# Performance work log

Measured on AMD Instinct MI355X. Metric: run time of the kernel, lower is better.

## Reference

```python
import jax, jax.numpy as jnp
import numpy as np

N, E, D, ATT = 20000, 5000, 128, 32
NUM_LAYERS = 4
LN_EPS = 1e-5
DEG_EPS = 1e-12

def setup_inputs() -> dict:
    key = jax.random.key(0)
    k1, k2, k3, k4 = jax.random.split(key, 4)
    node_embeddings = jax.random.normal(k1, (N, D), dtype=jnp.float32)
    hypergraph_matrix = (jax.random.uniform(k2, (N, E)) < 0.01).astype(jnp.float32)
    ln_gamma = jnp.ones((D,), jnp.float32)
    ln_beta = jnp.zeros((D,), jnp.float32)
    W_att = jax.random.normal(k3, (D, ATT), dtype=jnp.float32) * (1.0 / np.sqrt(D))
    b_att = jnp.zeros((ATT,), jnp.float32)
    q_att = jax.random.normal(k4, (ATT,), dtype=jnp.float32)
    return {"node_embeddings": node_embeddings, "hypergraph_matrix": hypergraph_matrix,
            "ln_gamma": ln_gamma, "ln_beta": ln_beta,
            "W_att": W_att, "b_att": b_att, "q_att": q_att}

def _layernorm(y, gamma, beta):
    mu = jnp.mean(y, axis=-1, keepdims=True)
    var = jnp.mean(jnp.square(y - mu), axis=-1, keepdims=True)
    return (y - mu) * jax.lax.rsqrt(var + LN_EPS) * gamma + beta

def reference(node_embeddings, hypergraph_matrix, ln_gamma, ln_beta, W_att, b_att, q_att):
    H = hypergraph_matrix                      # [N, E]
    dv_inv = 1.0 / jnp.maximum(jnp.sum(H, axis=1), DEG_EPS)   # [N]
    de_inv = 1.0 / jnp.maximum(jnp.sum(H, axis=0), DEG_EPS)   # [E]
    x = node_embeddings
    for _ in range(NUM_LAYERS):
        edge_mean = (H.T @ x) * de_inv[:, None]       # V->E mean, [E, D]
        node_msg = (H @ edge_mean) * dv_inv[:, None]  # E->V mean, [N, D]
        x = _layernorm(node_msg + node_embeddings, ln_gamma, ln_beta)
        # dropout(p=0.35) is identity in eval mode
    # per-edge masked mean over member nodes (vectorized segment-mean)
    M = (H > 0).astype(x.dtype)                        # [N, E]
    cnt = jnp.maximum(jnp.sum(M, axis=0), 1.0)         # [E]
    edge_out = (M.T @ x) / cnt[:, None]                # [E, D]
    # dot-product attention pooling over hyperedges
    scores = jax.nn.softmax(jnp.tanh(edge_out @ W_att + b_att) @ q_att)  # [E]
    return scores @ edge_out                           # [D]
```

## Files before the change

kernel.cpp:

```cpp
#include <hip/hip_runtime.h>
#include <hip/hip_bf16.h>
#include <hip/hip_fp16.h>
#include <math.h>

#define NN 20000
#define EE 5000
#define DD 128
#define ATT 32
#define NUM_LAYERS 4
#define LN_EPS 1e-5f
#define DEG_EPS 1e-12f

#define ECAP 320
#define NCAP 128

__device__ inline void acc4h(float4& a, uint2 u) {
    __half2 h0 = __builtin_bit_cast(__half2, u.x);
    __half2 h1 = __builtin_bit_cast(__half2, u.y);
    a.x += __low2float(h0); a.y += __high2float(h0);
    a.z += __low2float(h1); a.w += __high2float(h1);
}

__device__ inline uint2 pack4h(float x, float y, float z, float w) {
    uint2 u;
    u.x = __builtin_bit_cast(unsigned, __floats2half2_rn(x, y));
    u.y = __builtin_bit_cast(unsigned, __floats2half2_rn(z, w));
    return u;
}

__global__ __launch_bounds__(256) void build_lists(
    const float* __restrict__ H, int* __restrict__ ec, int* __restrict__ nc,
    int* __restrict__ el, int* __restrict__ nl) {
    const int n = blockIdx.x;
    const int tid = threadIdx.x;
    __shared__ int lcnt;
    if (tid == 0) lcnt = 0;
    __syncthreads();
    const float4* row = reinterpret_cast<const float4*>(H + (size_t)n * EE);
    for (int i = tid; i < EE / 4; i += 256) {
        float4 h = row[i];
        float v[4] = {h.x, h.y, h.z, h.w};
        const int ebase = i * 4;
#pragma unroll
        for (int k = 0; k < 4; k++) {
            if (v[k] != 0.0f) {
                const int e = ebase + k;
                int s = atomicAdd(&lcnt, 1);
                if (s < NCAP) nl[n * NCAP + s] = e;
                int se = atomicAdd(&ec[e], 1);
                if (se < ECAP) el[e * ECAP + se] = n;
            }
        }
    }
    __syncthreads();
    if (tid == 0) nc[n] = lcnt;
}

__global__ __launch_bounds__(256) void cvt_to_h(
    const float* __restrict__ src, __half* __restrict__ dst, int n4) {
    const int i = blockIdx.x * 256 + threadIdx.x;
    if (i >= n4) return;
    const float4 v = reinterpret_cast<const float4*>(src)[i];
    reinterpret_cast<uint2*>(dst)[i] = pack4h(v.x, v.y, v.z, v.w);
}

template <bool OUT_HALF>
__global__ __launch_bounds__(256) void edge_gather(
    const __half* __restrict__ xh, const int* __restrict__ ec,
    const int* __restrict__ el, void* __restrict__ out) {
    __shared__ float4 part[4][32];
    const int e = blockIdx.x;
    const int tid = threadIdx.x;
    const int wv = tid >> 6;
    const int lane = tid & 63;
    const int q = lane & 31;
    const int stream = wv * 2 + (lane >> 5);
    const int cnt = ec[e];
    const int c = min(cnt, ECAP);
    const int* lst = el + e * ECAP;
    float4 a0 = make_float4(0.f, 0.f, 0.f, 0.f);
    float4 a1 = make_float4(0.f, 0.f, 0.f, 0.f);
    int i = stream;
    for (; i + 8 < c; i += 16) {
        const int n0 = lst[i];
        const int n1 = lst[i + 8];
        const uint2 r0 = *reinterpret_cast<const uint2*>(xh + n0 * DD + (q << 2));
        const uint2 r1 = *reinterpret_cast<const uint2*>(xh + n1 * DD + (q << 2));
        acc4h(a0, r0);
        acc4h(a1, r1);
    }
    if (i < c) {
        const uint2 r0 = *reinterpret_cast<const uint2*>(xh + lst[i] * DD + (q << 2));
        acc4h(a0, r0);
    }
    a0.x += a1.x; a0.y += a1.y; a0.z += a1.z; a0.w += a1.w;
    a0.x += __shfl_down(a0.x, 32);
    a0.y += __shfl_down(a0.y, 32);
    a0.z += __shfl_down(a0.z, 32);
    a0.w += __shfl_down(a0.w, 32);
    if (lane < 32) part[wv][q] = a0;
    __syncthreads();
    if (tid < 32) {
        const float4 p0 = part[0][q];
        const float4 p1 = part[1][q];
        const float4 p2 = part[2][q];
        const float4 p3 = part[3][q];
        const float inv = 1.0f / fmaxf((float)cnt, DEG_EPS);
        const float ox = (p0.x + p1.x + p2.x + p3.x) * inv;
        const float oy = (p0.y + p1.y + p2.y + p3.y) * inv;
        const float oz = (p0.z + p1.z + p2.z + p3.z) * inv;
        const float ow = (p0.w + p1.w + p2.w + p3.w) * inv;
        if (OUT_HALF) {
            reinterpret_cast<uint2*>((__half*)out + e * DD)[q] = pack4h(ox, oy, oz, ow);
        } else {
            reinterpret_cast<float4*>((float*)out + e * DD)[q] = make_float4(ox, oy, oz, ow);
        }
    }
}

__global__ __launch_bounds__(128) void node_gather_ln(
    const __half* __restrict__ emean, const int* __restrict__ nc,
    const int* __restrict__ nl, const float* __restrict__ x0,
    const float* __restrict__ gamma, const float* __restrict__ beta,
    __half* __restrict__ xout) {
    __shared__ float4 part[2][32];
    const int n = blockIdx.x;
    const int tid = threadIdx.x;
    const int wv = tid >> 6;
    const int lane = tid & 63;
    const int q = lane & 31;
    const int stream = wv * 2 + (lane >> 5);
    const int cnt = nc[n];
    const int c = min(cnt, NCAP);
    const int* lst = nl + n * NCAP;
    float4 a0 = make_float4(0.f, 0.f, 0.f, 0.f);
    float4 a1 = make_float4(0.f, 0.f, 0.f, 0.f);
    int i = stream;
    for (; i + 4 < c; i += 8) {
        const int e0 = lst[i];
        const int e1 = lst[i + 4];
        const uint2 r0 = *reinterpret_cast<const uint2*>(emean + e0 * DD + (q << 2));
        const uint2 r1 = *reinterpret_cast<const uint2*>(emean + e1 * DD + (q << 2));
        acc4h(a0, r0);
        acc4h(a1, r1);
    }
    if (i < c) {
        const uint2 r0 = *reinterpret_cast<const uint2*>(emean + lst[i] * DD + (q << 2));
        acc4h(a0, r0);
    }
    a0.x += a1.x; a0.y += a1.y; a0.z += a1.z; a0.w += a1.w;
    a0.x += __shfl_down(a0.x, 32);
    a0.y += __shfl_down(a0.y, 32);
    a0.z += __shfl_down(a0.z, 32);
    a0.w += __shfl_down(a0.w, 32);
    if (lane < 32) part[wv][q] = a0;
    __syncthreads();
    if (tid < 64) {
        const float4 p0 = part[0][q];
        const float4 p1 = part[1][q];
        const float inv = 1.0f / fmaxf((float)cnt, DEG_EPS);
        const float4 x0v = *reinterpret_cast<const float4*>(x0 + n * DD + (q << 2));
        float4 y;
        y.x = (p0.x + p1.x) * inv + x0v.x;
        y.y = (p0.y + p1.y) * inv + x0v.y;
        y.z = (p0.z + p1.z) * inv + x0v.z;
        y.w = (p0.w + p1.w) * inv + x0v.w;
        float s = y.x + y.y + y.z + y.w;
        float ss = y.x * y.x + y.y * y.y + y.z * y.z + y.w * y.w;
        for (int off = 16; off > 0; off >>= 1) {
            s += __shfl_down(s, off);
            ss += __shfl_down(ss, off);
        }
        s = __shfl(s, 0);
        ss = __shfl(ss, 0);
        const float mu = s * (1.0f / 128.0f);
        float var = ss * (1.0f / 128.0f) - mu * mu;
        var = fmaxf(var, 0.0f);
        const float rstd = 1.0f / sqrtf(var + LN_EPS);
        if (lane < 32) {
            const float4 g = *reinterpret_cast<const float4*>(gamma + (q << 2));
            const float4 b = *reinterpret_cast<const float4*>(beta + (q << 2));
            const float ox = (y.x - mu) * rstd * g.x + b.x;
            const float oy = (y.y - mu) * rstd * g.y + b.y;
            const float oz = (y.z - mu) * rstd * g.z + b.z;
            const float ow = (y.w - mu) * rstd * g.w + b.w;
            reinterpret_cast<uint2*>(xout + n * DD)[q] = pack4h(ox, oy, oz, ow);
        }
    }
}

__global__ __launch_bounds__(128) void att_scores(
    const float* __restrict__ eout, const float* __restrict__ W,
    const float* __restrict__ b, const float* __restrict__ qv,
    float* __restrict__ t) {
    __shared__ float row[DD];
    const int e = blockIdx.x;
    const int tid = threadIdx.x;
    row[tid] = eout[e * DD + tid];
    __syncthreads();
    float r = 0.0f;
    if (tid < ATT) {
        float a = 0.0f;
#pragma unroll 4
        for (int d = 0; d < DD; d++) a += row[d] * W[d * ATT + tid];
        r = tanhf(a + b[tid]) * qv[tid];
    }
    for (int off = 16; off > 0; off >>= 1) r += __shfl_down(r, off);
    if (tid == 0) t[e] = r;
}

__global__ __launch_bounds__(1024) void softmax_stats(
    const float* __restrict__ t, float* __restrict__ MS) {
    __shared__ float red[16];
    __shared__ float smax;
    const int tid = threadIdx.x;
    const int wid = tid >> 6;
    float m = -1e30f;
    for (int i = tid; i < EE; i += 1024) m = fmaxf(m, t[i]);
    for (int off = 32; off > 0; off >>= 1) m = fmaxf(m, __shfl_down(m, off));
    if ((tid & 63) == 0) red[wid] = m;
    __syncthreads();
    if (tid < 64) {
        float v = (tid < 16) ? red[tid] : -1e30f;
        for (int off = 8; off > 0; off >>= 1) v = fmaxf(v, __shfl_down(v, off));
        if (tid == 0) smax = v;
    }
    __syncthreads();
    const float M = smax;
    float sum = 0.0f;
    for (int i = tid; i < EE; i += 1024) sum += expf(t[i] - M);
    for (int off = 32; off > 0; off >>= 1) sum += __shfl_down(sum, off);
    if ((tid & 63) == 0) red[wid] = sum;
    __syncthreads();
    if (tid < 64) {
        float v = (tid < 16) ? red[tid] : 0.0f;
        for (int off = 8; off > 0; off >>= 1) v += __shfl_down(v, off);
        if (tid == 0) { MS[0] = M; MS[1] = v; }
    }
}

__global__ __launch_bounds__(128) void weighted_sum(
    const float* __restrict__ eout, const float* __restrict__ t,
    const float* __restrict__ MS, float* __restrict__ out) {
    const int d = threadIdx.x;
    const float M = MS[0];
    const float invS = 1.0f / MS[1];
    float acc = 0.0f;
    for (int e = blockIdx.x; e < EE; e += gridDim.x) {
        const float w = expf(t[e] - M);
        acc += w * eout[e * DD + d];
    }
    atomicAdd(&out[d], acc * invS);
}

extern "C" void kernel_launch(void* const* d_in, const int* in_sizes, int n_in,
                              void* d_out, int out_size, void* d_ws, size_t ws_size,
                              hipStream_t stream) {
    const float* x0 = (const float*)d_in[0];
    const float* H = (const float*)d_in[1];
    const float* gamma = (const float*)d_in[2];
    const float* beta = (const float*)d_in[3];
    const float* W = (const float*)d_in[4];
    const float* b = (const float*)d_in[5];
    const float* qv = (const float*)d_in[6];
    float* out = (float*)d_out;

    char* w = (char*)d_ws;
    int* ec = (int*)w;       w += (size_t)EE * 4;
    int* nc = (int*)w;       w += (size_t)NN * 4;
    int* el = (int*)w;       w += (size_t)EE * ECAP * 4;
    int* nl = (int*)w;       w += (size_t)NN * NCAP * 4;
    __half* xh0 = (__half*)w; w += (size_t)NN * DD * 2;
    __half* xA = (__half*)w;  w += (size_t)NN * DD * 2;
    __half* xB = (__half*)w;  w += (size_t)NN * DD * 2;
    __half* emean = (__half*)w; w += (size_t)EE * DD * 2;
    float* eout = (float*)w; w += (size_t)EE * DD * 4;
    float* t = (float*)w;    w += (size_t)EE * 4;
    float* MS = (float*)w;   w += 16;

    hipMemsetAsync(d_ws, 0, (size_t)(EE + NN) * 4, stream);
    hipMemsetAsync(d_out, 0, (size_t)DD * sizeof(float), stream);

    build_lists<<<NN, 256, 0, stream>>>(H, ec, nc, el, nl);
    cvt_to_h<<<(NN * DD / 4 + 255) / 256, 256, 0, stream>>>(x0, xh0, NN * DD / 4);

    const __half* xin = xh0;
    __half* bufs[2] = {xA, xB};
    for (int l = 0; l < NUM_LAYERS; l++) {
        edge_gather<true><<<EE, 256, 0, stream>>>(xin, ec, el, emean);
        node_gather_ln<<<NN, 128, 0, stream>>>(emean, nc, nl, x0, gamma, beta, bufs[l & 1]);
        xin = bufs[l & 1];
    }

    edge_gather<false><<<EE, 256, 0, stream>>>(xin, ec, el, eout);
    att_scores<<<EE, 128, 0, stream>>>(eout, W, b, qv, t);
    softmax_stats<<<1, 1024, 0, stream>>>(t, MS);
    weighted_sum<<<64, 128, 0, stream>>>(eout, t, MS, out);
}
```

Before: 911.5 us.

## Split incidence list build into row and column passes, widen gathers to 16-byte loads

The single list-building kernel, which did global atomics per nonzero for the edge lists, becomes two kernels. A row pass builds node lists in shared memory. A column pass scans 16-column strips in 4 row chunks and builds edge lists with shared atomics plus one global atomic per column per chunk. The gather kernels now stage index lists in shared memory and use 16-byte half loads (8 features per lane), and the final edge gather is fused with the attention-score computation to drop a launch and an eout reread. The column pass reads H with strided 64-byte row segments, which may be less efficient, and H is now read twice.

```diff
diff --git a/kernel.cpp b/kernel.cpp
--- a/kernel.cpp
+++ b/kernel.cpp
@@ -1,5 +1,4 @@
 #include <hip/hip_runtime.h>
-#include <hip/hip_bf16.h>
 #include <hip/hip_fp16.h>
 #include <math.h>
 
@@ -14,26 +13,28 @@
 #define ECAP 320
 #define NCAP 128
 
-__device__ inline void acc4h(float4& a, uint2 u) {
-    __half2 h0 = __builtin_bit_cast(__half2, u.x);
-    __half2 h1 = __builtin_bit_cast(__half2, u.y);
-    a.x += __low2float(h0); a.y += __high2float(h0);
-    a.z += __low2float(h1); a.w += __high2float(h1);
-}
-
-__device__ inline uint2 pack4h(float x, float y, float z, float w) {
-    uint2 u;
-    u.x = __builtin_bit_cast(unsigned, __floats2half2_rn(x, y));
-    u.y = __builtin_bit_cast(unsigned, __floats2half2_rn(z, w));
-    return u;
-}
-
-__global__ __launch_bounds__(256) void build_lists(
-    const float* __restrict__ H, int* __restrict__ ec, int* __restrict__ nc,
-    int* __restrict__ el, int* __restrict__ nl) {
+#define CP_COLS 16
+#define CP_ROWCHUNK 5000
+#define CP_NCHUNKS ((EE + CP_COLS - 1) / CP_COLS)
+#define CP_CAP 128
+
+__device__ inline unsigned pack2h(float x, float y) {
+    return __builtin_bit_cast(unsigned, __floats2half2_rn(x, y));
+}
+__device__ inline void acc8(float* a, uint4 u) {
+    __half2 h;
+    h = __builtin_bit_cast(__half2, u.x); a[0] += __low2float(h); a[1] += __high2float(h);
+    h = __builtin_bit_cast(__half2, u.y); a[2] += __low2float(h); a[3] += __high2float(h);
+    h = __builtin_bit_cast(__half2, u.z); a[4] += __low2float(h); a[5] += __high2float(h);
+    h = __builtin_bit_cast(__half2, u.w); a[6] += __low2float(h); a[7] += __high2float(h);
+}
+
+__global__ __launch_bounds__(256) void rowpass_nl(
+    const float* __restrict__ H, int* __restrict__ nc, int* __restrict__ nl) {
     const int n = blockIdx.x;
     const int tid = threadIdx.x;
     __shared__ int lcnt;
+    __shared__ int lbuf[NCAP];
     if (tid == 0) lcnt = 0;
     __syncthreads();
     const float4* row = reinterpret_cast<const float4*>(H + (size_t)n * EE);
@@ -44,16 +45,65 @@
 #pragma unroll
         for (int k = 0; k < 4; k++) {
             if (v[k] != 0.0f) {
-                const int e = ebase + k;
                 int s = atomicAdd(&lcnt, 1);
-                if (s < NCAP) nl[n * NCAP + s] = e;
-                int se = atomicAdd(&ec[e], 1);
-                if (se < ECAP) el[e * ECAP + se] = n;
+                if (s < NCAP) lbuf[s] = ebase + k;
             }
         }
     }
     __syncthreads();
+    const int c = min(lcnt, NCAP);
+    for (int k = tid; k < c; k += 256) nl[(size_t)n * NCAP + k] = lbuf[k];
     if (tid == 0) nc[n] = lcnt;
+}
+
+__global__ __launch_bounds__(256) void colpass_el(
+    const float* __restrict__ H, int* __restrict__ ec, int* __restrict__ el) {
+    const int cchunk = blockIdx.x % CP_NCHUNKS;
+    const int rchunk = blockIdx.x / CP_NCHUNKS;
+    const int cbase = cchunk * CP_COLS;
+    const int cw = min(CP_COLS, EE - cbase);
+    const int r0 = rchunk * CP_ROWCHUNK;
+    __shared__ int lcnt[CP_COLS];
+    __shared__ int lbase[CP_COLS];
+    __shared__ int lists[CP_COLS][CP_CAP];
+    const int tid = threadIdx.x;
+    if (tid < CP_COLS) lcnt[tid] = 0;
+    __syncthreads();
+    for (int r = tid; r < CP_ROWCHUNK; r += 256) {
+        const int row = r0 + r;
+        const float* p = H + (size_t)row * EE + cbase;
+        float v[CP_COLS];
+        *reinterpret_cast<float4*>(v + 0) = *reinterpret_cast<const float4*>(p + 0);
+        *reinterpret_cast<float4*>(v + 4) = *reinterpret_cast<const float4*>(p + 4);
+        if (cw == CP_COLS) {
+            *reinterpret_cast<float4*>(v + 8)  = *reinterpret_cast<const float4*>(p + 8);
+            *reinterpret_cast<float4*>(v + 12) = *reinterpret_cast<const float4*>(p + 12);
+        }
+#pragma unroll
+        for (int j = 0; j < CP_COLS; j++) {
+            if (j < cw && v[j] != 0.0f) {
+                int s = atomicAdd(&lcnt[j], 1);
+                if (s < CP_CAP) lists[j][s] = row;
+            }
+        }
+    }
+    __syncthreads();
+    const int j = tid >> 4;
+    const int k0 = tid & 15;
+    if (j < cw) {
+        const int cnt = min(lcnt[j], CP_CAP);
+        if (k0 == 0) lbase[j] = atomicAdd(&ec[cbase + j], cnt);
+    }
+    __syncthreads();
+    if (j < cw) {
+        const int cnt = min(lcnt[j], CP_CAP);
+        const int base = lbase[j];
+        int* dst = el + (size_t)(cbase + j) * ECAP;
+        for (int k = k0; k < cnt; k += 16) {
+            const int idx = base + k;
+            if (idx < ECAP) dst[idx] = lists[j][k];
+        }
+    }
 }
 
 __global__ __launch_bounds__(256) void cvt_to_h(
@@ -61,152 +111,169 @@
     const int i = blockIdx.x * 256 + threadIdx.x;
     if (i >= n4) return;
     const float4 v = reinterpret_cast<const float4*>(src)[i];
-    reinterpret_cast<uint2*>(dst)[i] = pack4h(v.x, v.y, v.z, v.w);
-}
-
-template <bool OUT_HALF>
-__global__ __launch_bounds__(256) void edge_gather(
+    uint2 u; u.x = pack2h(v.x, v.y); u.y = pack2h(v.z, v.w);
+    reinterpret_cast<uint2*>(dst)[i] = u;
+}
+
+template <bool FINAL>
+__global__ __launch_bounds__(256) void edge_gather16(
     const __half* __restrict__ xh, const int* __restrict__ ec,
-    const int* __restrict__ el, void* __restrict__ out) {
-    __shared__ float4 part[4][32];
+    const int* __restrict__ el, __half* __restrict__ outh,
+    float* __restrict__ eout, const float* __restrict__ W,
+    const float* __restrict__ bb, const float* __restrict__ qv,
+    float* __restrict__ t) {
+    __shared__ int ilst[ECAP];
+    __shared__ float part[4][16][8];
+    __shared__ float rowbuf[DD];
     const int e = blockIdx.x;
     const int tid = threadIdx.x;
-    const int wv = tid >> 6;
-    const int lane = tid & 63;
-    const int q = lane & 31;
-    const int stream = wv * 2 + (lane >> 5);
     const int cnt = ec[e];
     const int c = min(cnt, ECAP);
-    const int* lst = el + e * ECAP;
-    float4 a0 = make_float4(0.f, 0.f, 0.f, 0.f);
-    float4 a1 = make_float4(0.f, 0.f, 0.f, 0.f);
-    int i = stream;
-    for (; i + 8 < c; i += 16) {
-        const int n0 = lst[i];
-        const int n1 = lst[i + 8];
-        const uint2 r0 = *reinterpret_cast<const uint2*>(xh + n0 * DD + (q << 2));
-        const uint2 r1 = *reinterpret_cast<const uint2*>(xh + n1 * DD + (q << 2));
-        acc4h(a0, r0);
-        acc4h(a1, r1);
+    const int* lst = el + (size_t)e * ECAP;
+    for (int k = tid; k < c; k += 256) ilst[k] = lst[k];
+    __syncthreads();
+    const int lane16 = tid & 15;
+    const int s = tid >> 4;
+    const int wave = tid >> 6;
+    float a[8] = {0, 0, 0, 0, 0, 0, 0, 0};
+    float b[8] = {0, 0, 0, 0, 0, 0, 0, 0};
+    int i = s;
+    for (; i + 16 < c; i += 32) {
+        const int n0 = ilst[i];
+        const int n1 = ilst[i + 16];
+        acc8(a, *reinterpret_cast<const uint4*>(xh + n0 * DD + lane16 * 8));
+        acc8(b, *reinterpret_cast<const uint4*>(xh + n1 * DD + lane16 * 8));
     }
     if (i < c) {
-        const uint2 r0 = *reinterpret_cast<const uint2*>(xh + lst[i] * DD + (q << 2));
-        acc4h(a0, r0);
-    }
-    a0.x += a1.x; a0.y += a1.y; a0.z += a1.z; a0.w += a1.w;
-    a0.x += __shfl_down(a0.x, 32);
-    a0.y += __shfl_down(a0.y, 32);
-    a0.z += __shfl_down(a0.z, 32);
-    a0.w += __shfl_down(a0.w, 32);
-    if (lane < 32) part[wv][q] = a0;
-    __syncthreads();
-    if (tid < 32) {
-        const float4 p0 = part[0][q];
-        const float4 p1 = part[1][q];
-        const float4 p2 = part[2][q];
-        const float4 p3 = part[3][q];
+        acc8(a, *reinterpret_cast<const uint4*>(xh + ilst[i] * DD + lane16 * 8));
+    }
+#pragma unroll
+    for (int k = 0; k < 8; k++) {
+        float v = a[k] + b[k];
+        v += __shfl_down(v, 16);
+        v += __shfl_down(v, 32);
+        a[k] = v;
+    }
+    if ((tid & 63) < 16) {
+#pragma unroll
+        for (int k = 0; k < 8; k++) part[wave][lane16][k] = a[k];
+    }
+    __syncthreads();
+    if (tid < 16) {
         const float inv = 1.0f / fmaxf((float)cnt, DEG_EPS);
-        const float ox = (p0.x + p1.x + p2.x + p3.x) * inv;
-        const float oy = (p0.y + p1.y + p2.y + p3.y) * inv;
-        const float oz = (p0.z + p1.z + p2.z + p3.z) * inv;
-        const float ow = (p0.w + p1.w + p2.w + p3.w) * inv;
-        if (OUT_HALF) {
-            reinterpret_cast<uint2*>((__half*)out + e * DD)[q] = pack4h(ox, oy, oz, ow);
+        float o[8];
+#pragma unroll
+        for (int k = 0; k < 8; k++)
+            o[k] = (part[0][tid][k] + part[1][tid][k] + part[2][tid][k] + part[3][tid][k]) * inv;
+        if (!FINAL) {
+            uint4 u;
+            u.x = pack2h(o[0], o[1]); u.y = pack2h(o[2], o[3]);
+            u.z = pack2h(o[4], o[5]); u.w = pack2h(o[6], o[7]);
+            *reinterpret_cast<uint4*>(outh + e * DD + tid * 8) = u;
         } else {
-            reinterpret_cast<float4*>((float*)out + e * DD)[q] = make_float4(ox, oy, oz, ow);
-        }
-    }
-}
-
-__global__ __launch_bounds__(128) void node_gather_ln(
+#pragma unroll
+            for (int k = 0; k < 8; k++) rowbuf[tid * 8 + k] = o[k];
+            *reinterpret_cast<float4*>(eout + e * DD + tid * 8) =
+                make_float4(o[0], o[1], o[2], o[3]);
+            *reinterpret_cast<float4*>(eout + e * DD + tid * 8 + 4) =
+                make_float4(o[4], o[5], o[6], o[7]);
+        }
+    }
+    if (FINAL) {
+        __syncthreads();
+        float r = 0.0f;
+        if (tid < ATT) {
+            float acc = 0.0f;
+#pragma unroll 4
+            for (int d = 0; d < DD; d++) acc += rowbuf[d] * W[d * ATT + tid];
+            r = tanhf(acc + bb[tid]) * qv[tid];
+        }
+        for (int off = 16; off > 0; off >>= 1) r += __shfl_down(r, off);
+        if (tid == 0) t[e] = r;
+    }
+}
+
+__global__ __launch_bounds__(128) void node_gather_ln16(
     const __half* __restrict__ emean, const int* __restrict__ nc,
     const int* __restrict__ nl, const float* __restrict__ x0,
     const float* __restrict__ gamma, const float* __restrict__ beta,
     __half* __restrict__ xout) {
-    __shared__ float4 part[2][32];
+    __shared__ int ilst[NCAP];
+    __shared__ float part[2][16][8];
     const int n = blockIdx.x;
     const int tid = threadIdx.x;
-    const int wv = tid >> 6;
-    const int lane = tid & 63;
-    const int q = lane & 31;
-    const int stream = wv * 2 + (lane >> 5);
     const int cnt = nc[n];
     const int c = min(cnt, NCAP);
-    const int* lst = nl + n * NCAP;
-    float4 a0 = make_float4(0.f, 0.f, 0.f, 0.f);
-    float4 a1 = make_float4(0.f, 0.f, 0.f, 0.f);
-    int i = stream;
-    for (; i + 4 < c; i += 8) {
-        const int e0 = lst[i];
-        const int e1 = lst[i + 4];
-        const uint2 r0 = *reinterpret_cast<const uint2*>(emean + e0 * DD + (q << 2));
-        const uint2 r1 = *reinterpret_cast<const uint2*>(emean + e1 * DD + (q << 2));
-        acc4h(a0, r0);
-        acc4h(a1, r1);
+    const int* lst = nl + (size_t)n * NCAP;
+    if (tid < c) ilst[tid] = lst[tid];
+    __syncthreads();
+    const int lane16 = tid & 15;
+    const int s = tid >> 4;
+    const int wave = tid >> 6;
+    float a[8] = {0, 0, 0, 0, 0, 0, 0, 0};
+    float b[8] = {0, 0, 0, 0, 0, 0, 0, 0};
+    int i = s;
+    for (; i + 8 < c; i += 16) {
+        const int e0 = ilst[i];
+        const int e1 = ilst[i + 8];
+        acc8(a, *reinterpret_cast<const uint4*>(emean + e0 * DD + lane16 * 8));
+        acc8(b, *reinterpret_cast<const uint4*>(emean + e1 * DD + lane16 * 8));
     }
     if (i < c) {
-        const uint2 r0 = *reinterpret_cast<const uint2*>(emean + lst[i] * DD + (q << 2));
-        acc4h(a0, r0);
-    }
-    a0.x += a1.x; a0.y += a1.y; a0.z += a1.z; a0.w += a1.w;
-    a0.x += __shfl_down(a0.x, 32);
-    a0.y += __shfl_down(a0.y, 32);
-    a0.z += __shfl_down(a0.z, 32);
-    a0.w += __shfl_down(a0.w, 32);
-    if (lane < 32) part[wv][q] = a0;
-    __syncthreads();
-    if (tid < 64) {
-        const float4 p0 = part[0][q];
-        const float4 p1 = part[1][q];
+        acc8(a, *reinterpret_cast<const uint4*>(emean + ilst[i] * DD + lane16 * 8));
+    }
+#pragma unroll
+    for (int k = 0; k < 8; k++) {
+        float v = a[k] + b[k];
+        v += __shfl_down(v, 16);
+        v += __shfl_down(v, 32);
+        a[k] = v;
+    }
+    if ((tid & 63) < 16) {
+#pragma unroll
+        for (int k = 0; k < 8; k++) part[wave][lane16][k] = a[k];
+    }
+    __syncthreads();
+    if (tid < 16) {
         const float inv = 1.0f / fmaxf((float)cnt, DEG_EPS);
-        const float4 x0v = *reinterpret_cast<const float4*>(x0 + n * DD + (q << 2));
-        float4 y;
-        y.x = (p0.x + p1.x) * inv + x0v.x;
-        y.y = (p0.y + p1.y) * inv + x0v.y;
-        y.z = (p0.z + p1.z) * inv + x0v.z;
-        y.w = (p0.w + p1.w) * inv + x0v.w;
-        float s = y.x + y.y + y.z + y.w;
-        float ss = y.x * y.x + y.y * y.y + y.z * y.z + y.w * y.w;
-        for (int off = 16; off > 0; off >>= 1) {
-            s += __shfl_down(s, off);
+        const float4 x0a = *reinterpret_cast<const float4*>(x0 + n * DD + tid * 8);
+        const float4 x0b = *reinterpret_cast<const float4*>(x0 + n * DD + tid * 8 + 4);
+        float y[8];
+        y[0] = (part[0][tid][0] + part[1][tid][0]) * inv + x0a.x;
+        y[1] = (part[0][tid][1] + part[1][tid][1]) * inv + x0a.y;
+        y[2] = (part[0][tid][2] + part[1][tid][2]) * inv + x0a.z;
+        y[3] = (part[0][tid][3] + part[1][tid][3]) * inv + x0a.w;
+        y[4] = (part[0][tid][4] + part[1][tid][4]) * inv + x0b.x;
+        y[5] = (part[0][tid][5] + part[1][tid][5]) * inv + x0b.y;
+        y[6] = (part[0][tid][6] + part[1][tid][6]) * inv + x0b.z;
+        y[7] = (part[0][tid][7] + part[1][tid][7]) * inv + x0b.w;
+        float sm = 0.0f, ss = 0.0f;
+#pragma unroll
+        for (int k = 0; k < 8; k++) { sm += y[k]; ss += y[k] * y[k]; }
+        for (int off = 8; off > 0; off >>= 1) {
+            sm += __shfl_down(sm, off);
             ss += __shfl_down(ss, off);
         }
-        s = __shfl(s, 0);
+        sm = __shfl(sm, 0);
         ss = __shfl(ss, 0);
-        const float mu = s * (1.0f / 128.0f);
+        const float mu = sm * (1.0f / 128.0f);
         float var = ss * (1.0f / 128.0f) - mu * mu;
         var = fmaxf(var, 0.0f);
         const float rstd = 1.0f / sqrtf(var + LN_EPS);
-        if (lane < 32) {
-            const float4 g = *reinterpret_cast<const float4*>(gamma + (q << 2));
-            const float4 b = *reinterpret_cast<const float4*>(beta + (q << 2));
-            const float ox = (y.x - mu) * rstd * g.x + b.x;
-            const float oy = (y.y - mu) * rstd * g.y + b.y;
-            const float oz = (y.z - mu) * rstd * g.z + b.z;
-            const float ow = (y.w - mu) * rstd * g.w + b.w;
-            reinterpret_cast<uint2*>(xout + n * DD)[q] = pack4h(ox, oy, oz, ow);
-        }
-    }
-}
-
-__global__ __launch_bounds__(128) void att_scores(
-    const float* __restrict__ eout, const float* __restrict__ W,
-    const float* __restrict__ b, const float* __restrict__ qv,
-    float* __restrict__ t) {
-    __shared__ float row[DD];
-    const int e = blockIdx.x;
-    const int tid = threadIdx.x;
-    row[tid] = eout[e * DD + tid];
-    __syncthreads();
-    float r = 0.0f;
-    if (tid < ATT) {
-        float a = 0.0f;
-#pragma unroll 4
-        for (int d = 0; d < DD; d++) a += row[d] * W[d * ATT + tid];
-        r = tanhf(a + b[tid]) * qv[tid];
-    }
-    for (int off = 16; off > 0; off >>= 1) r += __shfl_down(r, off);
-    if (tid == 0) t[e] = r;
+        const float4 g0 = *reinterpret_cast<const float4*>(gamma + tid * 8);
+        const float4 g1 = *reinterpret_cast<const float4*>(gamma + tid * 8 + 4);
+        const float4 b0 = *reinterpret_cast<const float4*>(beta + tid * 8);
+        const float4 b1 = *reinterpret_cast<const float4*>(beta + tid * 8 + 4);
+        float gg[8] = {g0.x, g0.y, g0.z, g0.w, g1.x, g1.y, g1.z, g1.w};
+        float bb[8] = {b0.x, b0.y, b0.z, b0.w, b1.x, b1.y, b1.z, b1.w};
+        float o[8];
+#pragma unroll
+        for (int k = 0; k < 8; k++) o[k] = (y[k] - mu) * rstd * gg[k] + bb[k];
+        uint4 u;
+        u.x = pack2h(o[0], o[1]); u.y = pack2h(o[2], o[3]);
+        u.z = pack2h(o[4], o[5]); u.w = pack2h(o[6], o[7]);
+        *reinterpret_cast<uint4*>(xout + n * DD + tid * 8) = u;
+    }
 }
 
 __global__ __launch_bounds__(1024) void softmax_stats(
@@ -266,34 +333,37 @@
     float* out = (float*)d_out;
 
     char* w = (char*)d_ws;
-    int* ec = (int*)w;       w += (size_t)EE * 4;
-    int* nc = (int*)w;       w += (size_t)NN * 4;
-    int* el = (int*)w;       w += (size_t)EE * ECAP * 4;
-    int* nl = (int*)w;       w += (size_t)NN * NCAP * 4;
+    int* ec = (int*)w;        w += (size_t)EE * 4;
+    int* nc = (int*)w;        w += (size_t)NN * 4;
+    int* el = (int*)w;        w += (size_t)EE * ECAP * 4;
+    int* nl = (int*)w;        w += (size_t)NN * NCAP * 4;
     __half* xh0 = (__half*)w; w += (size_t)NN * DD * 2;
     __half* xA = (__half*)w;  w += (size_t)NN * DD * 2;
     __half* xB = (__half*)w;  w += (size_t)NN * DD * 2;
     __half* emean = (__half*)w; w += (size_t)EE * DD * 2;
-    float* eout = (float*)w; w += (size_t)EE * DD * 4;
-    float* t = (float*)w;    w += (size_t)EE * 4;
-    float* MS = (float*)w;   w += 16;
-
-    hipMemsetAsync(d_ws, 0, (size_t)(EE + NN) * 4, stream);
+    float* eout = (float*)w;  w += (size_t)EE * DD * 4;
+    float* t = (float*)w;     w += (size_t)EE * 4;
+    float* MS = (float*)w;    w += 16;
+
+    hipMemsetAsync(ec, 0, (size_t)EE * 4, stream);
     hipMemsetAsync(d_out, 0, (size_t)DD * sizeof(float), stream);
 
-    build_lists<<<NN, 256, 0, stream>>>(H, ec, nc, el, nl);
+    rowpass_nl<<<NN, 256, 0, stream>>>(H, nc, nl);
+    colpass_el<<<CP_NCHUNKS * 4, 256, 0, stream>>>(H, ec, el);
     cvt_to_h<<<(NN * DD / 4 + 255) / 256, 256, 0, stream>>>(x0, xh0, NN * DD / 4);
 
     const __half* xin = xh0;
     __half* bufs[2] = {xA, xB};
     for (int l = 0; l < NUM_LAYERS; l++) {
-        edge_gather<true><<<EE, 256, 0, stream>>>(xin, ec, el, emean);
-        node_gather_ln<<<NN, 128, 0, stream>>>(emean, nc, nl, x0, gamma, beta, bufs[l & 1]);
+        edge_gather16<false><<<EE, 256, 0, stream>>>(
+            xin, ec, el, emean, nullptr, nullptr, nullptr, nullptr, nullptr);
+        node_gather_ln16<<<NN, 128, 0, stream>>>(
+            emean, nc, nl, x0, gamma, beta, bufs[l & 1]);
         xin = bufs[l & 1];
     }
 
-    edge_gather<false><<<EE, 256, 0, stream>>>(xin, ec, el, eout);
-    att_scores<<<EE, 128, 0, stream>>>(eout, W, b, qv, t);
+    edge_gather16<true><<<EE, 256, 0, stream>>>(
+        xin, ec, el, nullptr, eout, W, b, qv, t);
     softmax_stats<<<1, 1024, 0, stream>>>(t, MS);
     weighted_sum<<<64, 128, 0, stream>>>(eout, t, MS, out);
 }
```

Result: no change. 926.9 us (+1.7%).
